# Kernel tuning notes

Measured on AMD Instinct MI355X. Metric: run time of the kernel, lower is better.

The kernel has to match this reference:

```python
import jax, jax.numpy as jnp
import numpy as np
import math

CW = 10
T_S = 2.0


def _K(t0):
    t = t0 - CW // 2
    if t < 0:
        return -0.5 * math.exp(t / (T_S / 2.0))
    return math.exp(-t / T_S)

K_VALS = np.array([_K(k) for k in range(CW)], dtype=np.float32)          # synaptic kernel
KS_VALS = np.array([math.exp(-k / T_S) for k in range(CW)], dtype=np.float32)  # spike kernel


def swish(v):
    # original Swish: x * sigmoid(10*x)
    return v * jax.nn.sigmoid(10.0 * v)


def act_fun(v):
    # smooth surrogate spike activation: sigmoid(10*(mem - 0.5)), thresh=0.5
    return jax.nn.sigmoid(10.0 * (v - 0.5))


def setup_inputs() -> dict:
    key = jax.random.key(0)
    k1, k2, k3, k4 = jax.random.split(key, 4)
    B, T = 4096, 50
    x = jax.random.uniform(k1, (B, T, 620), dtype=jnp.float32)
    W1 = jax.random.normal(k2, (200, 620), dtype=jnp.float32) / np.sqrt(620.0)
    W2 = jax.random.normal(k3, (100, 200), dtype=jnp.float32) / np.sqrt(200.0)
    W3 = jax.random.normal(k4, (11, 100), dtype=jnp.float32) / np.sqrt(100.0)
    return {"x": x, "W1": W1, "W2": W2, "W3": W3}


def reference(x, W1, W2, W3):
    B, T, _ = x.shape
    kv = jnp.asarray(K_VALS)
    ks_tail = jnp.asarray(KS_VALS[1:])   # k=1..9; k=0 spike term is always 0 (buffer not yet written)
    kv_tail = jnp.asarray(K_VALS[1:])    # k=1..9 for layer-input history

    # h1 is purely feedforward in time -> precompute, then causal conv with K over CW window.
    h1 = swish(jnp.einsum('btd,nd->btn', x, W1))            # [B, T, 200]
    h1_pad = jnp.pad(h1, ((0, 0), (CW - 1, 0), (0, 0)))
    syn2 = sum(kv[k] * h1_pad[:, CW - 1 - k: CW - 1 - k + T] for k in range(CW))  # [B, T, 200]

    def shift(hist, new):
        # hist[:, j] holds value at time t-1-j; prepend current value
        return jnp.concatenate([new[:, None], hist[:, :-1]], axis=1)

    def step(carry, syn2_t):
        sl2_h, h2_h, sl3_h, h3_h, sl4_h, acc = carry
        # layer 2
        mem2 = syn2_t - jnp.einsum('k,bkn->bn', ks_tail, sl2_h)
        s2 = act_fun(mem2)
        sl2 = s2 * mem2
        h2 = swish(s2 @ W2.T)                                # [B, 100]
        # layer 3
        mem3 = kv[0] * h2 + jnp.einsum('k,bkn->bn', kv_tail, h2_h) \
               - jnp.einsum('k,bkn->bn', ks_tail, sl3_h)
        s3 = act_fun(mem3)
        sl3 = s3 * mem3
        h3 = swish(s3 @ W3.T)                                # [B, 11]
        # layer 4 (output)
        mem4 = kv[0] * h3 + jnp.einsum('k,bkn->bn', kv_tail, h3_h) \
               - jnp.einsum('k,bkn->bn', ks_tail, sl4_h)
        s4 = act_fun(mem4)
        sl4 = s4 * mem4
        carry = (shift(sl2_h, sl2), shift(h2_h, h2), shift(sl3_h, sl3),
                 shift(h3_h, h3), shift(sl4_h, sl4), acc + s4)
        return carry, None

    z = lambda n: jnp.zeros((B, CW - 1, n), dtype=x.dtype)
    carry0 = (z(200), z(100), z(100), z(11), z(11), jnp.zeros((B, 11), dtype=x.dtype))
    carry, _ = jax.lax.scan(step, carry0, jnp.swapaxes(syn2, 0, 1))
    h4_sumspike = carry[-1]
    return h4_sumspike / 50.0
```

## Files before the change

kernel.cpp:

```cpp
#include <hip/hip_runtime.h>
#include <math.h>

#define T_STEPS 50
#define D_IN    620
#define N1      200
#define N2      100
#define N3      11
#define BATCH   4096

typedef short bf16x8 __attribute__((ext_vector_type(8)));
typedef float f32x4  __attribute__((ext_vector_type(4)));

__device__ __constant__ float KV[10] = {
    -0.0033689735f, -0.0091578194f, -0.0248935342f, -0.0676676416f, -0.1839397206f,
     1.0f,           0.6065306597f,  0.3678794412f,  0.2231301601f,  0.1353352832f };
__device__ __constant__ float KS_TAIL[9] = {
    0.6065306597f, 0.3678794412f, 0.2231301601f, 0.1353352832f, 0.0820849986f,
    0.0497870684f, 0.0301973834f, 0.0183156389f, 0.0111089965f };

__device__ __forceinline__ float sigm10(float x) { return 1.0f / (1.0f + __expf(-10.0f * x)); }
__device__ __forceinline__ float swishf(float v) { return v / (1.0f + __expf(-10.0f * v)); }

__device__ __forceinline__ void split2(float x, unsigned short& hi, unsigned short& lo) {
    unsigned u = __float_as_uint(x);
    hi = (unsigned short)(u >> 16);
    float rem = x - __uint_as_float(u & 0xFFFF0000u);
    lo = (unsigned short)(__float_as_uint(rem) >> 16);
}

__global__ void prep_w1(const float* __restrict__ W1, unsigned short* __restrict__ W1pre) {
    int i = blockIdx.x * 256 + threadIdx.x;
    if (i >= 266240) return;
    int kk = i & 31;
    int t1 = i >> 5;
    int n  = t1 % 208;
    int t2 = t1 / 208;
    int p  = t2 & 1;
    int kt = t2 >> 1;
    int k  = kt * 32 + kk;
    float w = (n < N1 && k < D_IN) ? W1[n * D_IN + k] : 0.0f;
    unsigned short hi, lo; split2(w, hi, lo);
    int gsw = (kk >> 3) ^ ((n >> 1) & 3);
    int idx = kt * 13312 + p * 6656 + n * 32 + gsw * 8 + (kk & 7);
    W1pre[idx] = p ? lo : hi;
}

__global__ void prep_w2(const float* __restrict__ W2, unsigned short* __restrict__ W2pre2) {
    int i = blockIdx.x * 256 + threadIdx.x;
    if (i >= 57344) return;
    int e  = i & 7;
    int r  = i >> 3;
    int l  = r & 63;
    int r2 = r >> 6;
    int p  = r2 & 1;
    int r3 = r2 >> 1;
    int ks = r3 % 7;
    int wv = r3 / 7;
    int n  = wv * 16 + (l & 15);
    int k  = ks * 32 + (l >> 4) * 8 + e;
    float v = (n < N2 && k < N1) ? W2[n * N1 + k] : 0.0f;
    unsigned short hi, lo; split2(v, hi, lo);
    W2pre2[i] = p ? lo : hi;
}

__global__ __launch_bounds__(512, 4) void gemm1_mfma(const float* __restrict__ x,
                                                     const unsigned short* __restrict__ W1pre,
                                                     float* __restrict__ h1) {
    __shared__ unsigned short Bs[2][13312];

    const int tid = threadIdx.x;
    const int w   = tid >> 6;
    const int l   = tid & 63;
    const int j   = l >> 4;
    const int r16 = l & 15;
    const long row0 = (long)blockIdx.x * 128;
    const float* arow = x + (row0 + w * 16 + r16) * D_IN;

    f32x4 acc[13];
#pragma unroll
    for (int nt = 0; nt < 13; ++nt) acc[nt] = (f32x4){0.f, 0.f, 0.f, 0.f};

    auto stageB = [&](int kt, int bb) {
        const unsigned short* src = W1pre + kt * 13312;
#pragma unroll
        for (int it = 0; it < 3; ++it) {
            int ch = it * 512 + tid;
            __builtin_amdgcn_global_load_lds(
                (const __attribute__((address_space(1))) unsigned int*)(src + ch * 8),
                (__attribute__((address_space(3))) unsigned int*)(&Bs[bb][0] + ch * 8), 16, 0, 0);
        }
        if (tid < 128) {
            int ch = 1536 + tid;
            __builtin_amdgcn_global_load_lds(
                (const __attribute__((address_space(1))) unsigned int*)(src + ch * 8),
                (__attribute__((address_space(3))) unsigned int*)(&Bs[bb][0] + ch * 8), 16, 0, 0);
        }
    };

    auto loadA = [&](int kt, float* av) {
        const float* p = arow + kt * 32 + j * 8;
        const float4 u0 = *(const float4*)p;
        const float4 u1 = *(const float4*)(p + 4);
        av[0] = u0.x; av[1] = u0.y; av[2] = u0.z; av[3] = u0.w;
        av[4] = u1.x; av[5] = u1.y; av[6] = u1.z; av[7] = u1.w;
    };
    auto loadAtail = [&](float* av) {
        if (j == 0) {
            const float4 u0 = *(const float4*)(arow + 608);
            const float4 u1 = *(const float4*)(arow + 612);
            av[0] = u0.x; av[1] = u0.y; av[2] = u0.z; av[3] = u0.w;
            av[4] = u1.x; av[5] = u1.y; av[6] = u1.z; av[7] = u1.w;
        } else if (j == 1) {
            const float4 u0 = *(const float4*)(arow + 616);
            av[0] = u0.x; av[1] = u0.y; av[2] = u0.z; av[3] = u0.w;
            av[4] = 0.f; av[5] = 0.f; av[6] = 0.f; av[7] = 0.f;
        } else {
#pragma unroll
            for (int e = 0; e < 8; ++e) av[e] = 0.f;
        }
    };

    float avc[8], avn[8];
    stageB(0, 0);
    loadA(0, avc);
    __syncthreads();

    for (int kt = 0; kt < 20; ++kt) {
        const int cur = kt & 1, nxt = cur ^ 1;
        if (kt < 19) {
            stageB(kt + 1, nxt);
            if (kt + 1 == 19) loadAtail(avn); else loadA(kt + 1, avn);
        }
        bf16x8 ah, al;
#pragma unroll
        for (int e = 0; e < 8; ++e) {
            unsigned short hi, lo; split2(avc[e], hi, lo);
            ah[e] = (short)hi; al[e] = (short)lo;
        }
        const unsigned short* B = &Bs[cur][0];
#pragma unroll
        for (int nt = 0; nt < 13; ++nt) {
            const int n  = nt * 16 + r16;
            const int gs = j ^ ((n >> 1) & 3);
            const bf16x8 bh = *(const bf16x8*)(B + n * 32 + gs * 8);
            const bf16x8 bl = *(const bf16x8*)(B + 6656 + n * 32 + gs * 8);
            acc[nt] = __builtin_amdgcn_mfma_f32_16x16x32_bf16(ah, bh, acc[nt], 0, 0, 0);
            acc[nt] = __builtin_amdgcn_mfma_f32_16x16x32_bf16(ah, bl, acc[nt], 0, 0, 0);
            acc[nt] = __builtin_amdgcn_mfma_f32_16x16x32_bf16(al, bh, acc[nt], 0, 0, 0);
        }
        __syncthreads();
#pragma unroll
        for (int e = 0; e < 8; ++e) avc[e] = avn[e];
    }

#pragma unroll
    for (int nt = 0; nt < 13; ++nt) {
        const int gcol = nt * 16 + r16;
        if (gcol < N1) {
            const long grow0 = row0 + w * 16 + j * 4;
#pragma unroll
            for (int q = 0; q < 4; ++q)
                h1[(grow0 + q) * N1 + gcol] = swishf(acc[nt][q]);
        }
    }
}

__global__ __launch_bounds__(256) void conv_k(float* __restrict__ buf) {
    __shared__ float h1s[T_STEPS * N1];
    const int b = blockIdx.x, tid = threadIdx.x;
    float* p = buf + (size_t)b * (T_STEPS * N1);
    for (int i = tid; i < T_STEPS * N1 / 4; i += 256)
        ((float4*)h1s)[i] = ((const float4*)p)[i];
    __syncthreads();
    for (int i = tid; i < T_STEPS * N1; i += 256) {
        int t = i / N1, n = i - t * N1;
        float s = 0.0f;
#pragma unroll
        for (int k = 0; k < 10; ++k)
            if (k <= t) s = fmaf(KV[k], h1s[(t - k) * N1 + n], s);
        p[i] = s;
    }
}

__global__ __launch_bounds__(512, 2) void snn_scan4(const float* __restrict__ syn2,
                                                    const unsigned short* __restrict__ W2pre2,
                                                    const float* __restrict__ W3,
                                                    float* __restrict__ out) {
    __shared__ __align__(16) unsigned short s2A[8192];
    __shared__ __align__(16) float h2buf[8][132];
    __shared__ __align__(16) float s3buf[8][104];
    __shared__ __align__(16) float W3s[N3 * N2];

    const int tid = threadIdx.x;
    const int wv  = tid >> 6;
    const int l   = tid & 63;
    const int m16 = l & 15;
    const int j2  = l >> 4;
    const int g   = wv;
    const int c   = l;
    const long b  = (long)blockIdx.x * 8 + g;

    for (int i = tid; i < N3 * N2; i += 512) W3s[i] = W3[i];
    for (int i = tid; i < 8192; i += 512) s2A[i] = 0;

    bf16x8 bh[7], bl[7];
    {
        const unsigned short* wp = W2pre2 + wv * 7168 + l * 8;
#pragma unroll
        for (int ks = 0; ks < 7; ++ks) {
            bh[ks] = *(const bf16x8*)(wp + ks * 1024);
            bl[ks] = *(const bf16x8*)(wp + ks * 1024 + 512);
        }
    }

    const int NL2 = (c < 8)  ? 4 : 3;
    const int NL3 = (c < 36) ? 2 : 1;

    float sl2h[9][4] = {};
    float h2h[9][2]  = {};
    float sl3h[9][2] = {};
    float h3h[9]     = {};
    float sl4h[9]    = {};
    float accum      = 0.0f;

    const float* syn2b = syn2 + b * (T_STEPS * N1);
    float syn_nxt[4];
#pragma unroll
    for (int j = 0; j < 4; ++j) syn_nxt[j] = (j < NL2) ? syn2b[c + 64 * j] : 0.0f;

    __syncthreads();

    for (int t = 0; t < T_STEPS; ++t) {
        float syn_cur[4];
#pragma unroll
        for (int j = 0; j < 4; ++j) syn_cur[j] = syn_nxt[j];
        if (t + 1 < T_STEPS) {
#pragma unroll
            for (int j = 0; j < 4; ++j)
                if (j < NL2) syn_nxt[j] = syn2b[(t + 1) * N1 + c + 64 * j];
        }

#pragma unroll
        for (int j = 0; j < 4; ++j) {
            if (j < NL2) {
                const int n = c + 64 * j;
                float mem2 = syn_cur[j];
#pragma unroll
                for (int k = 0; k < 9; ++k) mem2 = fmaf(-KS_TAIL[k], sl2h[k][j], mem2);
                const float s2  = sigm10(mem2 - 0.5f);
                const float sl2 = s2 * mem2;
#pragma unroll
                for (int k = 8; k > 0; --k) sl2h[k][j] = sl2h[k - 1][j];
                sl2h[0][j] = sl2;
                unsigned short hi, lo; split2(s2, hi, lo);
                const int off = g * 256 + (((n >> 3) ^ (g & 7)) * 8) + (n & 7);
                s2A[off]        = hi;
                s2A[4096 + off] = lo;
            }
        }
        __syncthreads();

        {
            f32x4 a0 = (f32x4){0.f, 0.f, 0.f, 0.f};
            f32x4 a1 = (f32x4){0.f, 0.f, 0.f, 0.f};
            const int swz = m16 & 7;
#pragma unroll
            for (int ks = 0; ks < 7; ++ks) {
                const int gr = (4 * ks + j2) ^ swz;
                const bf16x8 ahv = *(const bf16x8*)&s2A[m16 * 256 + gr * 8];
                const bf16x8 alv = *(const bf16x8*)&s2A[4096 + m16 * 256 + gr * 8];
                if (ks & 1) {
                    a1 = __builtin_amdgcn_mfma_f32_16x16x32_bf16(ahv, bh[ks], a1, 0, 0, 0);
                    a1 = __builtin_amdgcn_mfma_f32_16x16x32_bf16(alv, bh[ks], a1, 0, 0, 0);
                    a1 = __builtin_amdgcn_mfma_f32_16x16x32_bf16(ahv, bl[ks], a1, 0, 0, 0);
                } else {
                    a0 = __builtin_amdgcn_mfma_f32_16x16x32_bf16(ahv, bh[ks], a0, 0, 0, 0);
                    a0 = __builtin_amdgcn_mfma_f32_16x16x32_bf16(alv, bh[ks], a0, 0, 0, 0);
                    a0 = __builtin_amdgcn_mfma_f32_16x16x32_bf16(ahv, bl[ks], a0, 0, 0, 0);
                }
            }
            const f32x4 a = a0 + a1;
            if (j2 < 2) {
#pragma unroll
                for (int q = 0; q < 4; ++q)
                    h2buf[j2 * 4 + q][wv * 16 + m16] = swishf(a[q]);
            }
        }
        __syncthreads();

#pragma unroll
        for (int j = 0; j < 2; ++j) {
            if (j < NL3) {
                const int m = c + 64 * j;
                const float hm = h2buf[g][m];
                float mem3 = KV[0] * hm;
#pragma unroll
                for (int k = 0; k < 9; ++k) mem3 = fmaf(KV[k + 1], h2h[k][j], mem3);
#pragma unroll
                for (int k = 0; k < 9; ++k) mem3 = fmaf(-KS_TAIL[k], sl3h[k][j], mem3);
                const float s3  = sigm10(mem3 - 0.5f);
                const float sl3 = s3 * mem3;
#pragma unroll
                for (int k = 8; k > 0; --k) { h2h[k][j] = h2h[k - 1][j]; sl3h[k][j] = sl3h[k - 1][j]; }
                h2h[0][j]  = hm;
                sl3h[0][j] = sl3;
                s3buf[g][m] = s3;
            }
        }
        asm volatile("s_waitcnt lgkmcnt(0)" ::: "memory");
        __builtin_amdgcn_sched_barrier(0);

        if (c < N3) {
            float a4 = 0.0f;
#pragma unroll 5
            for (int m = 0; m < N2; m += 4) {
                const float4 sv  = *(const float4*)&s3buf[g][m];
                const float4 wv4 = *(const float4*)&W3s[c * N2 + m];
                a4 = fmaf(sv.x, wv4.x, a4);
                a4 = fmaf(sv.y, wv4.y, a4);
                a4 = fmaf(sv.z, wv4.z, a4);
                a4 = fmaf(sv.w, wv4.w, a4);
            }
            const float h3 = swishf(a4);
            float mem4 = KV[0] * h3;
#pragma unroll
            for (int k = 0; k < 9; ++k) mem4 = fmaf(KV[k + 1], h3h[k], mem4);
#pragma unroll
            for (int k = 0; k < 9; ++k) mem4 = fmaf(-KS_TAIL[k], sl4h[k], mem4);
            const float s4  = sigm10(mem4 - 0.5f);
            const float sl4 = s4 * mem4;
#pragma unroll
            for (int k = 8; k > 0; --k) { h3h[k] = h3h[k - 1]; sl4h[k] = sl4h[k - 1]; }
            h3h[0]  = h3;
            sl4h[0] = sl4;
            accum += s4;
        }
    }

    if (c < N3) out[b * N3 + c] = accum * 0.02f;
}

extern "C" void kernel_launch(void* const* d_in, const int* in_sizes, int n_in,
                              void* d_out, int out_size, void* d_ws, size_t ws_size,
                              hipStream_t stream) {
    const float* x  = (const float*)d_in[0];
    const float* W1 = (const float*)d_in[1];
    const float* W2 = (const float*)d_in[2];
    const float* W3 = (const float*)d_in[3];
    float* out = (float*)d_out;

    float* buf = (float*)d_ws;
    unsigned short* W1pre  = (unsigned short*)(buf + (size_t)BATCH * T_STEPS * N1);
    unsigned short* W2pre2 = W1pre + 266240;

    prep_w1<<<1040, 256, 0, stream>>>(W1, W1pre);
    prep_w2<<<224, 256, 0, stream>>>(W2, W2pre2);
    gemm1_mfma<<<(BATCH * T_STEPS) / 128, 512, 0, stream>>>(x, W1pre, buf);
    conv_k<<<BATCH, 256, 0, stream>>>(buf);
    snn_scan4<<<BATCH / 8, 512, 0, stream>>>(buf, W2pre2, W3, out);
}
```

Baseline: 646.3 us.

## Retile GEMM1 into N-split 2x7 tiles and recurse kernel sums in SNN scan

GEMM1 now has each 256-thread block cover half of the 200 output columns (112 padded) across 128 rows. Each wave computes a 2x7 tile of 16x16 MFMA blocks, and the k-loop is manually double-buffered. The SNN scan swaps the 9-tap history dot products for first-order recursive accumulators based on the exponential kernel (rho, rho^5, rho^10 corrections) over a ring buffer, unrolled by 10 time steps. The layer-4 reduction over 100 inputs is split across 44 threads plus a small shared-memory partial sum. In exchange, x is now read twice because of the N split, and the recursive sums can change float rounding.

```diff
diff --git a/kernel.cpp b/kernel.cpp
--- a/kernel.cpp
+++ b/kernel.cpp
@@ -14,9 +14,15 @@
 __device__ __constant__ float KV[10] = {
     -0.0033689735f, -0.0091578194f, -0.0248935342f, -0.0676676416f, -0.1839397206f,
      1.0f,           0.6065306597f,  0.3678794412f,  0.2231301601f,  0.1353352832f };
-__device__ __constant__ float KS_TAIL[9] = {
-    0.6065306597f, 0.3678794412f, 0.2231301601f, 0.1353352832f, 0.0820849986f,
-    0.0497870684f, 0.0301973834f, 0.0183156389f, 0.0111089965f };
+
+#define RHO    0.60653066f
+#define RHO5   0.0820849986f
+#define RHO10  0.0067379470f
+#define KV0    (-0.0033689735f)
+#define C1     (-0.0091578194f)
+#define C2     (-0.0248935342f)
+#define C3     (-0.0676676416f)
+#define C4     (-0.1839397206f)
 
 __device__ __forceinline__ float sigm10(float x) { return 1.0f / (1.0f + __expf(-10.0f * x)); }
 __device__ __forceinline__ float swishf(float v) { return v / (1.0f + __expf(-10.0f * v)); }
@@ -30,18 +36,20 @@
 
 __global__ void prep_w1(const float* __restrict__ W1, unsigned short* __restrict__ W1pre) {
     int i = blockIdx.x * 256 + threadIdx.x;
-    if (i >= 266240) return;
+    if (i >= 286720) return;
     int kk = i & 31;
     int t1 = i >> 5;
-    int n  = t1 % 208;
-    int t2 = t1 / 208;
+    int r  = t1 % 112;
+    int t2 = t1 / 112;
     int p  = t2 & 1;
-    int kt = t2 >> 1;
+    int nb = (t2 >> 1) & 1;
+    int kt = t2 >> 2;
+    int n  = nb * 112 + r;
     int k  = kt * 32 + kk;
     float w = (n < N1 && k < D_IN) ? W1[n * D_IN + k] : 0.0f;
     unsigned short hi, lo; split2(w, hi, lo);
-    int gsw = (kk >> 3) ^ ((n >> 1) & 3);
-    int idx = kt * 13312 + p * 6656 + n * 32 + gsw * 8 + (kk & 7);
+    int gsw = (kk >> 3) ^ ((r >> 1) & 3);
+    int idx = kt * 14336 + nb * 7168 + p * 3584 + r * 32 + gsw * 8 + (kk & 7);
     W1pre[idx] = p ? lo : hi;
 }
 
@@ -63,104 +71,123 @@
     W2pre2[i] = p ? lo : hi;
 }
 
-__global__ __launch_bounds__(512, 4) void gemm1_mfma(const float* __restrict__ x,
+__global__ __launch_bounds__(256, 4) void gemm1_mfma(const float* __restrict__ x,
                                                      const unsigned short* __restrict__ W1pre,
                                                      float* __restrict__ h1) {
-    __shared__ unsigned short Bs[2][13312];
+    __shared__ unsigned short Bs[2][7168];
 
     const int tid = threadIdx.x;
     const int w   = tid >> 6;
     const int l   = tid & 63;
     const int j   = l >> 4;
     const int r16 = l & 15;
-    const long row0 = (long)blockIdx.x * 128;
-    const float* arow = x + (row0 + w * 16 + r16) * D_IN;
-
-    f32x4 acc[13];
-#pragma unroll
-    for (int nt = 0; nt < 13; ++nt) acc[nt] = (f32x4){0.f, 0.f, 0.f, 0.f};
+    const int mb  = blockIdx.x >> 1;
+    const int nb  = blockIdx.x & 1;
+    const long row0 = (long)mb * 128;
+    const float* arow0 = x + (row0 + w * 32 + r16) * D_IN;
+    const float* arow1 = arow0 + 16 * D_IN;
+
+    f32x4 acc[2][7];
+#pragma unroll
+    for (int mt = 0; mt < 2; ++mt)
+#pragma unroll
+        for (int nt = 0; nt < 7; ++nt) acc[mt][nt] = (f32x4){0.f, 0.f, 0.f, 0.f};
 
     auto stageB = [&](int kt, int bb) {
-        const unsigned short* src = W1pre + kt * 13312;
+        const unsigned short* src = W1pre + kt * 14336 + nb * 7168;
 #pragma unroll
         for (int it = 0; it < 3; ++it) {
-            int ch = it * 512 + tid;
+            int ch = it * 256 + tid;
             __builtin_amdgcn_global_load_lds(
                 (const __attribute__((address_space(1))) unsigned int*)(src + ch * 8),
                 (__attribute__((address_space(3))) unsigned int*)(&Bs[bb][0] + ch * 8), 16, 0, 0);
         }
         if (tid < 128) {
-            int ch = 1536 + tid;
+            int ch = 768 + tid;
             __builtin_amdgcn_global_load_lds(
                 (const __attribute__((address_space(1))) unsigned int*)(src + ch * 8),
                 (__attribute__((address_space(3))) unsigned int*)(&Bs[bb][0] + ch * 8), 16, 0, 0);
         }
     };
 
-    auto loadA = [&](int kt, float* av) {
-        const float* p = arow + kt * 32 + j * 8;
-        const float4 u0 = *(const float4*)p;
-        const float4 u1 = *(const float4*)(p + 4);
-        av[0] = u0.x; av[1] = u0.y; av[2] = u0.z; av[3] = u0.w;
-        av[4] = u1.x; av[5] = u1.y; av[6] = u1.z; av[7] = u1.w;
+    auto loadA = [&](int kt, float (&av)[2][8]) {
+#pragma unroll
+        for (int mt = 0; mt < 2; ++mt) {
+            const float* ar = mt ? arow1 : arow0;
+            if (kt < 19) {
+                const float* p = ar + kt * 32 + j * 8;
+                const float4 u0 = *(const float4*)p;
+                const float4 u1 = *(const float4*)(p + 4);
+                av[mt][0] = u0.x; av[mt][1] = u0.y; av[mt][2] = u0.z; av[mt][3] = u0.w;
+                av[mt][4] = u1.x; av[mt][5] = u1.y; av[mt][6] = u1.z; av[mt][7] = u1.w;
+            } else if (j == 0) {
+                const float4 u0 = *(const float4*)(ar + 608);
+                const float4 u1 = *(const float4*)(ar + 612);
+                av[mt][0] = u0.x; av[mt][1] = u0.y; av[mt][2] = u0.z; av[mt][3] = u0.w;
+                av[mt][4] = u1.x; av[mt][5] = u1.y; av[mt][6] = u1.z; av[mt][7] = u1.w;
+            } else if (j == 1) {
+                const float4 u0 = *(const float4*)(ar + 616);
+                av[mt][0] = u0.x; av[mt][1] = u0.y; av[mt][2] = u0.z; av[mt][3] = u0.w;
+                av[mt][4] = 0.f; av[mt][5] = 0.f; av[mt][6] = 0.f; av[mt][7] = 0.f;
+            } else {
+#pragma unroll
+                for (int e = 0; e < 8; ++e) av[mt][e] = 0.f;
+            }
+        }
     };
-    auto loadAtail = [&](float* av) {
-        if (j == 0) {
-            const float4 u0 = *(const float4*)(arow + 608);
-            const float4 u1 = *(const float4*)(arow + 612);
-            av[0] = u0.x; av[1] = u0.y; av[2] = u0.z; av[3] = u0.w;
-            av[4] = u1.x; av[5] = u1.y; av[6] = u1.z; av[7] = u1.w;
-        } else if (j == 1) {
-            const float4 u0 = *(const float4*)(arow + 616);
-            av[0] = u0.x; av[1] = u0.y; av[2] = u0.z; av[3] = u0.w;
-            av[4] = 0.f; av[5] = 0.f; av[6] = 0.f; av[7] = 0.f;
-        } else {
-#pragma unroll
-            for (int e = 0; e < 8; ++e) av[e] = 0.f;
-        }
-    };
-
-    float avc[8], avn[8];
-    stageB(0, 0);
-    loadA(0, avc);
-    __syncthreads();
-
-    for (int kt = 0; kt < 20; ++kt) {
-        const int cur = kt & 1, nxt = cur ^ 1;
-        if (kt < 19) {
-            stageB(kt + 1, nxt);
-            if (kt + 1 == 19) loadAtail(avn); else loadA(kt + 1, avn);
-        }
-        bf16x8 ah, al;
-#pragma unroll
-        for (int e = 0; e < 8; ++e) {
-            unsigned short hi, lo; split2(avc[e], hi, lo);
-            ah[e] = (short)hi; al[e] = (short)lo;
-        }
+
+    auto computeKt = [&](float (&av)[2][8], int cur) {
+        bf16x8 ah[2], al[2];
+#pragma unroll
+        for (int mt = 0; mt < 2; ++mt)
+#pragma unroll
+            for (int e = 0; e < 8; ++e) {
+                unsigned short hi, lo; split2(av[mt][e], hi, lo);
+                ah[mt][e] = (short)hi; al[mt][e] = (short)lo;
+            }
         const unsigned short* B = &Bs[cur][0];
 #pragma unroll
-        for (int nt = 0; nt < 13; ++nt) {
+        for (int nt = 0; nt < 7; ++nt) {
             const int n  = nt * 16 + r16;
             const int gs = j ^ ((n >> 1) & 3);
             const bf16x8 bh = *(const bf16x8*)(B + n * 32 + gs * 8);
-            const bf16x8 bl = *(const bf16x8*)(B + 6656 + n * 32 + gs * 8);
-            acc[nt] = __builtin_amdgcn_mfma_f32_16x16x32_bf16(ah, bh, acc[nt], 0, 0, 0);
-            acc[nt] = __builtin_amdgcn_mfma_f32_16x16x32_bf16(ah, bl, acc[nt], 0, 0, 0);
-            acc[nt] = __builtin_amdgcn_mfma_f32_16x16x32_bf16(al, bh, acc[nt], 0, 0, 0);
-        }
+            const bf16x8 bl = *(const bf16x8*)(B + 3584 + n * 32 + gs * 8);
+            acc[0][nt] = __builtin_amdgcn_mfma_f32_16x16x32_bf16(ah[0], bh, acc[0][nt], 0, 0, 0);
+            acc[1][nt] = __builtin_amdgcn_mfma_f32_16x16x32_bf16(ah[1], bh, acc[1][nt], 0, 0, 0);
+            acc[0][nt] = __builtin_amdgcn_mfma_f32_16x16x32_bf16(ah[0], bl, acc[0][nt], 0, 0, 0);
+            acc[1][nt] = __builtin_amdgcn_mfma_f32_16x16x32_bf16(ah[1], bl, acc[1][nt], 0, 0, 0);
+            acc[0][nt] = __builtin_amdgcn_mfma_f32_16x16x32_bf16(al[0], bh, acc[0][nt], 0, 0, 0);
+            acc[1][nt] = __builtin_amdgcn_mfma_f32_16x16x32_bf16(al[1], bh, acc[1][nt], 0, 0, 0);
+        }
+    };
+
+    float avA[2][8], avB[2][8];
+    stageB(0, 0);
+    loadA(0, avA);
+    __syncthreads();
+
+#pragma unroll 1
+    for (int kt = 0; kt < 20; kt += 2) {
+        stageB(kt + 1, 1);
+        loadA(kt + 1, avB);
+        computeKt(avA, 0);
         __syncthreads();
-#pragma unroll
-        for (int e = 0; e < 8; ++e) avc[e] = avn[e];
+        if (kt + 2 < 20) { stageB(kt + 2, 0); loadA(kt + 2, avA); }
+        computeKt(avB, 1);
+        __syncthreads();
     }
 
 #pragma unroll
-    for (int nt = 0; nt < 13; ++nt) {
-        const int gcol = nt * 16 + r16;
-        if (gcol < N1) {
-            const long grow0 = row0 + w * 16 + j * 4;
-#pragma unroll
-            for (int q = 0; q < 4; ++q)
-                h1[(grow0 + q) * N1 + gcol] = swishf(acc[nt][q]);
+    for (int mt = 0; mt < 2; ++mt) {
+        const long grow0 = row0 + w * 32 + mt * 16 + j * 4;
+#pragma unroll
+        for (int nt = 0; nt < 7; ++nt) {
+            const int gcol = nb * 112 + nt * 16 + r16;
+            if (gcol < N1) {
+#pragma unroll
+                for (int q = 0; q < 4; ++q)
+                    h1[(grow0 + q) * N1 + gcol] = swishf(acc[mt][nt][q]);
+            }
         }
     }
 }
@@ -182,7 +209,7 @@
     }
 }
 
-__global__ __launch_bounds__(512, 2) void snn_scan4(const float* __restrict__ syn2,
+__global__ __launch_bounds__(512, 2) void snn_scan5(const float* __restrict__ syn2,
                                                     const unsigned short* __restrict__ W2pre2,
                                                     const float* __restrict__ W3,
                                                     float* __restrict__ out) {
@@ -190,6 +217,7 @@
     __shared__ __align__(16) float h2buf[8][132];
     __shared__ __align__(16) float s3buf[8][104];
     __shared__ __align__(16) float W3s[N3 * N2];
+    __shared__ __align__(16) float pbuf[8][4][12];
 
     const int tid = threadIdx.x;
     const int wv  = tid >> 6;
@@ -215,125 +243,151 @@
 
     const int NL2 = (c < 8)  ? 4 : 3;
     const int NL3 = (c < 36) ? 2 : 1;
-
-    float sl2h[9][4] = {};
-    float h2h[9][2]  = {};
-    float sl3h[9][2] = {};
-    float h3h[9]     = {};
-    float sl4h[9]    = {};
-    float accum      = 0.0f;
+    const int o4  = c % 11;
+    const int p4  = c / 11;
+    const int kbeg = (p4 == 0) ? 0 : (4 + 24 * p4);
+    const int nf4  = (p4 == 0) ? 7 : 6;
+
+    float sl2h[10][4] = {}; float Ssl2[4] = {};
+    float h2h[10][2]  = {}; float Dd3[2]  = {};
+    float sl3h[10][2] = {}; float Ssl3[2] = {};
+    float h3h[10]     = {}; float Dd4 = 0.f;
+    float sl4h[10]    = {}; float Ssl4 = 0.f;
+    float accum       = 0.0f;
 
     const float* syn2b = syn2 + b * (T_STEPS * N1);
     float syn_nxt[4];
 #pragma unroll
-    for (int j = 0; j < 4; ++j) syn_nxt[j] = (j < NL2) ? syn2b[c + 64 * j] : 0.0f;
+    for (int jj = 0; jj < 4; ++jj) syn_nxt[jj] = (jj < NL2) ? syn2b[c + 64 * jj] : 0.0f;
 
     __syncthreads();
 
-    for (int t = 0; t < T_STEPS; ++t) {
-        float syn_cur[4];
-#pragma unroll
-        for (int j = 0; j < 4; ++j) syn_cur[j] = syn_nxt[j];
-        if (t + 1 < T_STEPS) {
-#pragma unroll
-            for (int j = 0; j < 4; ++j)
-                if (j < NL2) syn_nxt[j] = syn2b[(t + 1) * N1 + c + 64 * j];
-        }
-
-#pragma unroll
-        for (int j = 0; j < 4; ++j) {
-            if (j < NL2) {
-                const int n = c + 64 * j;
-                float mem2 = syn_cur[j];
-#pragma unroll
-                for (int k = 0; k < 9; ++k) mem2 = fmaf(-KS_TAIL[k], sl2h[k][j], mem2);
-                const float s2  = sigm10(mem2 - 0.5f);
-                const float sl2 = s2 * mem2;
-#pragma unroll
-                for (int k = 8; k > 0; --k) sl2h[k][j] = sl2h[k - 1][j];
-                sl2h[0][j] = sl2;
-                unsigned short hi, lo; split2(s2, hi, lo);
-                const int off = g * 256 + (((n >> 3) ^ (g & 7)) * 8) + (n & 7);
-                s2A[off]        = hi;
-                s2A[4096 + off] = lo;
-            }
-        }
-        __syncthreads();
-
-        {
-            f32x4 a0 = (f32x4){0.f, 0.f, 0.f, 0.f};
-            f32x4 a1 = (f32x4){0.f, 0.f, 0.f, 0.f};
-            const int swz = m16 & 7;
-#pragma unroll
-            for (int ks = 0; ks < 7; ++ks) {
-                const int gr = (4 * ks + j2) ^ swz;
-                const bf16x8 ahv = *(const bf16x8*)&s2A[m16 * 256 + gr * 8];
-                const bf16x8 alv = *(const bf16x8*)&s2A[4096 + m16 * 256 + gr * 8];
-                if (ks & 1) {
-                    a1 = __builtin_amdgcn_mfma_f32_16x16x32_bf16(ahv, bh[ks], a1, 0, 0, 0);
-                    a1 = __builtin_amdgcn_mfma_f32_16x16x32_bf16(alv, bh[ks], a1, 0, 0, 0);
-                    a1 = __builtin_amdgcn_mfma_f32_16x16x32_bf16(ahv, bl[ks], a1, 0, 0, 0);
-                } else {
-                    a0 = __builtin_amdgcn_mfma_f32_16x16x32_bf16(ahv, bh[ks], a0, 0, 0, 0);
-                    a0 = __builtin_amdgcn_mfma_f32_16x16x32_bf16(alv, bh[ks], a0, 0, 0, 0);
-                    a0 = __builtin_amdgcn_mfma_f32_16x16x32_bf16(ahv, bl[ks], a0, 0, 0, 0);
+#pragma unroll 1
+    for (int tb = 0; tb < T_STEPS; tb += 10) {
+#pragma unroll
+        for (int u = 0; u < 10; ++u) {
+            const int t   = tb + u;
+            const int um1 = (u + 9) % 10;
+            const int um2 = (u + 8) % 10;
+            const int um3 = (u + 7) % 10;
+            const int um4 = (u + 6) % 10;
+            const int um5 = (u + 5) % 10;
+
+            float syn_cur[4];
+#pragma unroll
+            for (int jj = 0; jj < 4; ++jj) syn_cur[jj] = syn_nxt[jj];
+            if (t + 1 < T_STEPS) {
+#pragma unroll
+                for (int jj = 0; jj < 4; ++jj)
+                    if (jj < NL2) syn_nxt[jj] = syn2b[(t + 1) * N1 + c + 64 * jj];
+            }
+
+#pragma unroll
+            for (int jj = 0; jj < 4; ++jj) {
+                if (jj < NL2) {
+                    const int n = c + 64 * jj;
+                    const float slp = sl2h[um1][jj];
+                    const float slo = sl2h[u][jj];
+                    Ssl2[jj] = RHO * (Ssl2[jj] + slp) - RHO10 * slo;
+                    const float mem2 = syn_cur[jj] - Ssl2[jj];
+                    const float s2   = sigm10(mem2 - 0.5f);
+                    sl2h[u][jj] = s2 * mem2;
+                    unsigned short hi, lo; split2(s2, hi, lo);
+                    const int off = g * 256 + (((n >> 3) ^ (g & 7)) * 8) + (n & 7);
+                    s2A[off]        = hi;
+                    s2A[4096 + off] = lo;
                 }
             }
-            const f32x4 a = a0 + a1;
-            if (j2 < 2) {
-#pragma unroll
-                for (int q = 0; q < 4; ++q)
-                    h2buf[j2 * 4 + q][wv * 16 + m16] = swishf(a[q]);
-            }
-        }
-        __syncthreads();
-
-#pragma unroll
-        for (int j = 0; j < 2; ++j) {
-            if (j < NL3) {
-                const int m = c + 64 * j;
-                const float hm = h2buf[g][m];
-                float mem3 = KV[0] * hm;
-#pragma unroll
-                for (int k = 0; k < 9; ++k) mem3 = fmaf(KV[k + 1], h2h[k][j], mem3);
-#pragma unroll
-                for (int k = 0; k < 9; ++k) mem3 = fmaf(-KS_TAIL[k], sl3h[k][j], mem3);
-                const float s3  = sigm10(mem3 - 0.5f);
-                const float sl3 = s3 * mem3;
-#pragma unroll
-                for (int k = 8; k > 0; --k) { h2h[k][j] = h2h[k - 1][j]; sl3h[k][j] = sl3h[k - 1][j]; }
-                h2h[0][j]  = hm;
-                sl3h[0][j] = sl3;
-                s3buf[g][m] = s3;
-            }
-        }
-        asm volatile("s_waitcnt lgkmcnt(0)" ::: "memory");
-        __builtin_amdgcn_sched_barrier(0);
-
-        if (c < N3) {
-            float a4 = 0.0f;
-#pragma unroll 5
-            for (int m = 0; m < N2; m += 4) {
-                const float4 sv  = *(const float4*)&s3buf[g][m];
-                const float4 wv4 = *(const float4*)&W3s[c * N2 + m];
-                a4 = fmaf(sv.x, wv4.x, a4);
-                a4 = fmaf(sv.y, wv4.y, a4);
-                a4 = fmaf(sv.z, wv4.z, a4);
-                a4 = fmaf(sv.w, wv4.w, a4);
-            }
-            const float h3 = swishf(a4);
-            float mem4 = KV[0] * h3;
-#pragma unroll
-            for (int k = 0; k < 9; ++k) mem4 = fmaf(KV[k + 1], h3h[k], mem4);
-#pragma unroll
-            for (int k = 0; k < 9; ++k) mem4 = fmaf(-KS_TAIL[k], sl4h[k], mem4);
-            const float s4  = sigm10(mem4 - 0.5f);
-            const float sl4 = s4 * mem4;
-#pragma unroll
-            for (int k = 8; k > 0; --k) { h3h[k] = h3h[k - 1]; sl4h[k] = sl4h[k - 1]; }
-            h3h[0]  = h3;
-            sl4h[0] = sl4;
-            accum += s4;
+            __syncthreads();
+
+            {
+                f32x4 a0 = (f32x4){0.f, 0.f, 0.f, 0.f};
+                f32x4 a1 = (f32x4){0.f, 0.f, 0.f, 0.f};
+                const int swz = m16 & 7;
+#pragma unroll
+                for (int ks = 0; ks < 7; ++ks) {
+                    const int gr = (4 * ks + j2) ^ swz;
+                    const bf16x8 ahv = *(const bf16x8*)&s2A[m16 * 256 + gr * 8];
+                    const bf16x8 alv = *(const bf16x8*)&s2A[4096 + m16 * 256 + gr * 8];
+                    if (ks & 1) {
+                        a1 = __builtin_amdgcn_mfma_f32_16x16x32_bf16(ahv, bh[ks], a1, 0, 0, 0);
+                        a1 = __builtin_amdgcn_mfma_f32_16x16x32_bf16(alv, bh[ks], a1, 0, 0, 0);
+                        a1 = __builtin_amdgcn_mfma_f32_16x16x32_bf16(ahv, bl[ks], a1, 0, 0, 0);
+                    } else {
+                        a0 = __builtin_amdgcn_mfma_f32_16x16x32_bf16(ahv, bh[ks], a0, 0, 0, 0);
+                        a0 = __builtin_amdgcn_mfma_f32_16x16x32_bf16(alv, bh[ks], a0, 0, 0, 0);
+                        a0 = __builtin_amdgcn_mfma_f32_16x16x32_bf16(ahv, bl[ks], a0, 0, 0, 0);
+                    }
+                }
+                const f32x4 a = a0 + a1;
+                if (j2 < 2) {
+#pragma unroll
+                    for (int q = 0; q < 4; ++q)
+                        h2buf[j2 * 4 + q][wv * 16 + m16] = swishf(a[q]);
+                }
+            }
+            __syncthreads();
+
+#pragma unroll
+            for (int jj = 0; jj < 2; ++jj) {
+                if (jj < NL3) {
+                    const int m = c + 64 * jj;
+                    const float hm = h2buf[g][m];
+                    float gneg = C1 * h2h[um1][jj];
+                    gneg = fmaf(C2, h2h[um2][jj], gneg);
+                    gneg = fmaf(C3, h2h[um3][jj], gneg);
+                    gneg = fmaf(C4, h2h[um4][jj], gneg);
+                    Dd3[jj] = fmaf(RHO, Dd3[jj], h2h[um5][jj]);
+                    Dd3[jj] = fmaf(-RHO5, h2h[u][jj], Dd3[jj]);
+                    const float slp = sl3h[um1][jj];
+                    const float slo = sl3h[u][jj];
+                    Ssl3[jj] = RHO * (Ssl3[jj] + slp) - RHO10 * slo;
+                    const float mem3 = fmaf(KV0, hm, gneg) + Dd3[jj] - Ssl3[jj];
+                    const float s3   = sigm10(mem3 - 0.5f);
+                    sl3h[u][jj] = s3 * mem3;
+                    h2h[u][jj]  = hm;
+                    s3buf[g][m] = s3;
+                }
+            }
+            asm volatile("s_waitcnt lgkmcnt(0)" ::: "memory");
+            __builtin_amdgcn_sched_barrier(0);
+
+            if (c < 44) {
+                float part = 0.0f;
+#pragma unroll
+                for (int i = 0; i < 7; ++i) {
+                    if (i < nf4) {
+                        const float4 sv  = *(const float4*)&s3buf[g][kbeg + 4 * i];
+                        const float4 wv4 = *(const float4*)&W3s[o4 * N2 + kbeg + 4 * i];
+                        part = fmaf(sv.x, wv4.x, part);
+                        part = fmaf(sv.y, wv4.y, part);
+                        part = fmaf(sv.z, wv4.z, part);
+                        part = fmaf(sv.w, wv4.w, part);
+                    }
+                }
+                pbuf[g][p4][o4] = part;
+            }
+            asm volatile("s_waitcnt lgkmcnt(0)" ::: "memory");
+            __builtin_amdgcn_sched_barrier(0);
+
+            if (c < N3) {
+                const float a4 = pbuf[g][0][c] + pbuf[g][1][c] + pbuf[g][2][c] + pbuf[g][3][c];
+                const float h3 = swishf(a4);
+                float gneg = C1 * h3h[um1];
+                gneg = fmaf(C2, h3h[um2], gneg);
+                gneg = fmaf(C3, h3h[um3], gneg);
+                gneg = fmaf(C4, h3h[um4], gneg);
+                Dd4 = fmaf(RHO, Dd4, h3h[um5]);
+                Dd4 = fmaf(-RHO5, h3h[u], Dd4);
+                const float slp = sl4h[um1];
+                const float slo = sl4h[u];
+                Ssl4 = RHO * (Ssl4 + slp) - RHO10 * slo;
+                const float mem4 = fmaf(KV0, h3, gneg) + Dd4 - Ssl4;
+                const float s4   = sigm10(mem4 - 0.5f);
+                sl4h[u] = s4 * mem4;
+                h3h[u]  = h3;
+                accum += s4;
+            }
         }
     }
 
@@ -351,11 +405,11 @@
 
     float* buf = (float*)d_ws;
     unsigned short* W1pre  = (unsigned short*)(buf + (size_t)BATCH * T_STEPS * N1);
-    unsigned short* W2pre2 = W1pre + 266240;
-
-    prep_w1<<<1040, 256, 0, stream>>>(W1, W1pre);
+    unsigned short* W2pre2 = W1pre + 286720;
+
+    prep_w1<<<1120, 256, 0, stream>>>(W1, W1pre);
     prep_w2<<<224, 256, 0, stream>>>(W2, W2pre2);
-    gemm1_mfma<<<(BATCH * T_STEPS) / 128, 512, 0, stream>>>(x, W1pre, buf);
+    gemm1_mfma<<<3200, 256, 0, stream>>>(x, W1pre, buf);
     conv_k<<<BATCH, 256, 0, stream>>>(buf);
-    snn_scan4<<<BATCH / 8, 512, 0, stream>>>(buf, W2pre2, W3, out);
-}
+    snn_scan5<<<BATCH / 8, 512, 0, stream>>>(buf, W2pre2, W3, out);
+}
```

Result: faster. 582.4 us (-9.9%).
